# Kernel optimization log

Hardware: AMD Instinct MI355X
Metric: run time of the kernel (lower is better)

Reference implementation:

```python
import jax, jax.numpy as jnp
import numpy as np

N, I, O = 256, 1024, 1024

def setup_inputs() -> dict:
    key = jax.random.key(0)
    k1, k2, k3, k4 = jax.random.split(key, 4)
    x = jax.random.normal(k1, (N, I), dtype=jnp.float32)
    # attention acts as a soft drop-connect mask in [0, 1)
    attention = jax.random.uniform(k2, (N, I, O), dtype=jnp.float32)
    # kaiming-ish init scale for a linear layer
    weight = jax.random.normal(k3, (O, I), dtype=jnp.float32) * (1.0 / np.sqrt(I))
    bias_param = jax.random.normal(k4, (O,), dtype=jnp.float32) * 0.01
    return {"x": x, "attention": attention, "weight": weight, "bias_param": bias_param}

def reference(x, attention, weight, bias_param):
    # Per-sample attention-modulated linear:
    # out[n, o] = sum_i x[n, i] * weight[o, i] * attention[n, i, o] + bias[o]
    # Single fused contraction; never materializes the [N, O, I] modulated weight.
    out = jnp.einsum('ni,oi,nio->no', x, weight, attention)
    return out + bias_param
```

## Files before the change

kernel.cpp:

```cpp
#include <hip/hip_runtime.h>


typedef float f32x4 __attribute__((ext_vector_type(4)));

constexpr int Nn = 256;
constexpr int Ii = 1024;
constexpr int Oo = 1024;
constexpr int ISPLIT = 8;
constexpr int IRANGE = Ii / ISPLIT;
constexpr int TPB = 256;

__global__ __launch_bounds__(256)
void transpose_w_kernel(const float* __restrict__ w, float* __restrict__ wT) {
    __shared__ float tile[32][33];
    const int bi = blockIdx.x * 32;
    const int bo = blockIdx.y * 32;
    const int tx = threadIdx.x % 32;
    const int ty = threadIdx.x / 32;
    #pragma unroll
    for (int r = 0; r < 4; ++r)
        tile[ty + 8 * r][tx] = w[(size_t)(bo + ty + 8 * r) * Ii + bi + tx];
    __syncthreads();
    #pragma unroll
    for (int r = 0; r < 4; ++r)
        wT[(size_t)(bi + ty + 8 * r) * Oo + bo + tx] = tile[tx][ty + 8 * r];
}

__global__ __launch_bounds__(TPB)
void attn_partial_kernel(const float* __restrict__ x,
                         const float* __restrict__ att,
                         const float* __restrict__ wT,
                         float* __restrict__ partial) {
    __shared__ float xs[IRANGE];

    const int s   = blockIdx.x;
    const int n   = blockIdx.y;
    const int tid = threadIdx.x;
    const int i0  = s * IRANGE;

    if (tid < IRANGE / 4) {
        reinterpret_cast<f32x4*>(xs)[tid] =
            reinterpret_cast<const f32x4*>(x + (size_t)n * Ii + i0)[tid];
    }
    __syncthreads();

    const int o0 = tid * 4;
    const float* attp = att + ((size_t)n * Ii + i0) * Oo + o0;
    const float* wtp  = wT + (size_t)i0 * Oo + o0;

    f32x4 acc = {0.f, 0.f, 0.f, 0.f};

#define STEP(k, wV, aV)                                   \
    acc[0] = fmaf(xv[k] * wV[0], aV[0], acc[0]);          \
    acc[1] = fmaf(xv[k] * wV[1], aV[1], acc[1]);          \
    acc[2] = fmaf(xv[k] * wV[2], aV[2], acc[2]);          \
    acc[3] = fmaf(xv[k] * wV[3], aV[3], acc[3]);

    #pragma unroll 2
    for (int i = 0; i < IRANGE; i += 4) {
        f32x4 w0 = *reinterpret_cast<const f32x4*>(wtp + (size_t)(i + 0) * Oo);
        f32x4 w1 = *reinterpret_cast<const f32x4*>(wtp + (size_t)(i + 1) * Oo);
        f32x4 w2 = *reinterpret_cast<const f32x4*>(wtp + (size_t)(i + 2) * Oo);
        f32x4 w3 = *reinterpret_cast<const f32x4*>(wtp + (size_t)(i + 3) * Oo);
        f32x4 xv = *reinterpret_cast<const f32x4*>(&xs[i]);
        f32x4 a0 = __builtin_nontemporal_load(
            reinterpret_cast<const f32x4*>(attp + (size_t)(i + 0) * Oo));
        f32x4 a1 = __builtin_nontemporal_load(
            reinterpret_cast<const f32x4*>(attp + (size_t)(i + 1) * Oo));
        f32x4 a2 = __builtin_nontemporal_load(
            reinterpret_cast<const f32x4*>(attp + (size_t)(i + 2) * Oo));
        f32x4 a3 = __builtin_nontemporal_load(
            reinterpret_cast<const f32x4*>(attp + (size_t)(i + 3) * Oo));

        STEP(0, w0, a0)
        STEP(1, w1, a1)
        STEP(2, w2, a2)
        STEP(3, w3, a3)
    }
#undef STEP

    *reinterpret_cast<f32x4*>(partial + ((size_t)s * Nn + n) * Oo + o0) = acc;
}

__global__ __launch_bounds__(TPB)
void attn_reduce_kernel(const float* __restrict__ partial,
                        const float* __restrict__ bias,
                        float* __restrict__ out) {
    const int n   = blockIdx.x;
    const int tid = threadIdx.x;
    const int o0  = tid * 4;

    f32x4 acc = *reinterpret_cast<const f32x4*>(bias + o0);
    #pragma unroll
    for (int s = 0; s < ISPLIT; ++s) {
        f32x4 p = *reinterpret_cast<const f32x4*>(
            partial + ((size_t)s * Nn + n) * Oo + o0);
        acc[0] += p[0]; acc[1] += p[1]; acc[2] += p[2]; acc[3] += p[3];
    }
    *reinterpret_cast<f32x4*>(out + (size_t)n * Oo + o0) = acc;
}

extern "C" void kernel_launch(void* const* d_in, const int* in_sizes, int n_in,
                              void* d_out, int out_size, void* d_ws, size_t ws_size,
                              hipStream_t stream) {
    const float* x    = (const float*)d_in[0];
    const float* att  = (const float*)d_in[1];
    const float* w    = (const float*)d_in[2];
    const float* bias = (const float*)d_in[3];
    float* out        = (float*)d_out;

    float* partial = (float*)d_ws;
    float* wT      = (float*)((char*)d_ws + (size_t)ISPLIT * Nn * Oo * sizeof(float));

    dim3 tgrid(Ii / 32, Oo / 32);
    transpose_w_kernel<<<tgrid, 256, 0, stream>>>(w, wT);

    dim3 grid1(ISPLIT, Nn);
    attn_partial_kernel<<<grid1, TPB, 0, stream>>>(x, att, wT, partial);

    attn_reduce_kernel<<<Nn, TPB, 0, stream>>>(partial, bias, out);
}
```

Measured before the change: 202.2 us.

## Process four samples per block to reuse transposed weight loads

Each block of the partial kernel now handles four samples instead of one. It loads each transposed-weight vector once and applies it to four attention streams, so weight traffic drops by a factor of four. The grid shrinks to a quarter as many blocks, which cuts parallelism. Each thread also keeps more accumulators and more loads in flight. The kernel is dominated by the 1 GiB attention stream, so the saving on weight reads may be small next to that.

After: 191.5 us. 5.3% less time.

```diff
diff --git a/kernel.cpp b/kernel.cpp
--- a/kernel.cpp
+++ b/kernel.cpp
@@ -8,6 +8,7 @@
 constexpr int Oo = 1024;
 constexpr int ISPLIT = 8;
 constexpr int IRANGE = Ii / ISPLIT;
+constexpr int NB = 4;
 constexpr int TPB = 256;
 
 __global__ __launch_bounds__(256)
@@ -31,55 +32,67 @@
                          const float* __restrict__ att,
                          const float* __restrict__ wT,
                          float* __restrict__ partial) {
-    __shared__ float xs[IRANGE];
+    __shared__ float xs4[IRANGE][NB];
 
     const int s   = blockIdx.x;
-    const int n   = blockIdx.y;
+    const int ng  = blockIdx.y;
     const int tid = threadIdx.x;
     const int i0  = s * IRANGE;
+    const int n0  = ng * NB;
 
-    if (tid < IRANGE / 4) {
-        reinterpret_cast<f32x4*>(xs)[tid] =
-            reinterpret_cast<const f32x4*>(x + (size_t)n * Ii + i0)[tid];
+    if (tid < IRANGE) {
+        #pragma unroll
+        for (int j = 0; j < NB; ++j)
+            xs4[tid][j] = x[(size_t)(n0 + j) * Ii + i0 + tid];
     }
     __syncthreads();
 
     const int o0 = tid * 4;
-    const float* attp = att + ((size_t)n * Ii + i0) * Oo + o0;
-    const float* wtp  = wT + (size_t)i0 * Oo + o0;
+    const float* a0p = att + ((size_t)(n0 + 0) * Ii + i0) * Oo + o0;
+    const float* a1p = att + ((size_t)(n0 + 1) * Ii + i0) * Oo + o0;
+    const float* a2p = att + ((size_t)(n0 + 2) * Ii + i0) * Oo + o0;
+    const float* a3p = att + ((size_t)(n0 + 3) * Ii + i0) * Oo + o0;
+    const float* wtp = wT + (size_t)i0 * Oo + o0;
 
-    f32x4 acc = {0.f, 0.f, 0.f, 0.f};
+    f32x4 acc0 = {0.f, 0.f, 0.f, 0.f};
+    f32x4 acc1 = {0.f, 0.f, 0.f, 0.f};
+    f32x4 acc2 = {0.f, 0.f, 0.f, 0.f};
+    f32x4 acc3 = {0.f, 0.f, 0.f, 0.f};
 
-#define STEP(k, wV, aV)                                   \
-    acc[0] = fmaf(xv[k] * wV[0], aV[0], acc[0]);          \
-    acc[1] = fmaf(xv[k] * wV[1], aV[1], acc[1]);          \
-    acc[2] = fmaf(xv[k] * wV[2], aV[2], acc[2]);          \
-    acc[3] = fmaf(xv[k] * wV[3], aV[3], acc[3]);
+#define ROW(ii)                                                              \
+    {                                                                        \
+        const size_t roff = (size_t)(ii) * Oo;                               \
+        f32x4 wv = *reinterpret_cast<const f32x4*>(wtp + roff);              \
+        f32x4 xv = *reinterpret_cast<const f32x4*>(&xs4[ii][0]);             \
+        f32x4 b0 = __builtin_nontemporal_load(                               \
+            reinterpret_cast<const f32x4*>(a0p + roff));                     \
+        f32x4 b1 = __builtin_nontemporal_load(                               \
+            reinterpret_cast<const f32x4*>(a1p + roff));                     \
+        f32x4 b2 = __builtin_nontemporal_load(                               \
+            reinterpret_cast<const f32x4*>(a2p + roff));                     \
+        f32x4 b3 = __builtin_nontemporal_load(                               \
+            reinterpret_cast<const f32x4*>(a3p + roff));                     \
+        _Pragma("unroll")                                                    \
+        for (int k = 0; k < 4; ++k) {                                        \
+            acc0[k] = fmaf(xv[0] * wv[k], b0[k], acc0[k]);                   \
+            acc1[k] = fmaf(xv[1] * wv[k], b1[k], acc1[k]);                   \
+            acc2[k] = fmaf(xv[2] * wv[k], b2[k], acc2[k]);                   \
+            acc3[k] = fmaf(xv[3] * wv[k], b3[k], acc3[k]);                   \
+        }                                                                    \
+    }
 
     #pragma unroll 2
-    for (int i = 0; i < IRANGE; i += 4) {
-        f32x4 w0 = *reinterpret_cast<const f32x4*>(wtp + (size_t)(i + 0) * Oo);
-        f32x4 w1 = *reinterpret_cast<const f32x4*>(wtp + (size_t)(i + 1) * Oo);
-        f32x4 w2 = *reinterpret_cast<const f32x4*>(wtp + (size_t)(i + 2) * Oo);
-        f32x4 w3 = *reinterpret_cast<const f32x4*>(wtp + (size_t)(i + 3) * Oo);
-        f32x4 xv = *reinterpret_cast<const f32x4*>(&xs[i]);
-        f32x4 a0 = __builtin_nontemporal_load(
-            reinterpret_cast<const f32x4*>(attp + (size_t)(i + 0) * Oo));
-        f32x4 a1 = __builtin_nontemporal_load(
-            reinterpret_cast<const f32x4*>(attp + (size_t)(i + 1) * Oo));
-        f32x4 a2 = __builtin_nontemporal_load(
-            reinterpret_cast<const f32x4*>(attp + (size_t)(i + 2) * Oo));
-        f32x4 a3 = __builtin_nontemporal_load(
-            reinterpret_cast<const f32x4*>(attp + (size_t)(i + 3) * Oo));
+    for (int i = 0; i < IRANGE; i += 2) {
+        ROW(i + 0)
+        ROW(i + 1)
+    }
+#undef ROW
 
-        STEP(0, w0, a0)
-        STEP(1, w1, a1)
-        STEP(2, w2, a2)
-        STEP(3, w3, a3)
-    }
-#undef STEP
-
-    *reinterpret_cast<f32x4*>(partial + ((size_t)s * Nn + n) * Oo + o0) = acc;
+    float* pp = partial + ((size_t)s * Nn + n0) * Oo + o0;
+    *reinterpret_cast<f32x4*>(pp + 0 * (size_t)Oo) = acc0;
+    *reinterpret_cast<f32x4*>(pp + 1 * (size_t)Oo) = acc1;
+    *reinterpret_cast<f32x4*>(pp + 2 * (size_t)Oo) = acc2;
+    *reinterpret_cast<f32x4*>(pp + 3 * (size_t)Oo) = acc3;
 }
 
 __global__ __launch_bounds__(TPB)
@@ -115,7 +128,7 @@
     dim3 tgrid(Ii / 32, Oo / 32);
     transpose_w_kernel<<<tgrid, 256, 0, stream>>>(w, wT);
 
-    dim3 grid1(ISPLIT, Nn);
+    dim3 grid1(ISPLIT, Nn / NB);
     attn_partial_kernel<<<grid1, TPB, 0, stream>>>(x, att, wT, partial);
 
     attn_reduce_kernel<<<Nn, TPB, 0, stream>>>(partial, bias, out);
```
